# Optimization experiments

Hardware: AMD Instinct MI355X
Metric: run time of the kernel (lower is better)

Reference implementation:

```python
import jax, jax.numpy as jnp
import numpy as np


def setup_inputs() -> dict:
    key = jax.random.key(0)
    kq, kk, kv = jax.random.split(key, 3)
    B, S, D = 4, 4096, 128
    return {
        "q_proj": jax.random.normal(kq, (B, S, D), dtype=jnp.float32),
        "k_proj": jax.random.normal(kk, (B, S, D), dtype=jnp.float32),
        "v_proj": jax.random.normal(kv, (B, S, D), dtype=jnp.float32),
    }


def reference(q_proj, k_proj, v_proj):
    # Block-wise online softmax in the original is mathematically exact
    # full (non-causal) scaled dot-product attention.
    d = q_proj.shape[-1]
    scale = 1.0 / jnp.sqrt(jnp.asarray(d, dtype=q_proj.dtype))
    logits = jnp.einsum('bqd,bkd->bqk', q_proj, k_proj) * scale  # [B,S,S]
    attn = jax.nn.softmax(logits, axis=-1)
    return jnp.einsum('bqk,bkd->bqd', attn, v_proj)
```

## Files before the change

kernel.cpp:

```cpp
#include <hip/hip_runtime.h>
#include <hip/hip_bf16.h>
#include <stdint.h>

#define Bn 4
#define Sn 4096
#define Dn 128
#define SCALE ((float)(0.08838834764831843 * 1.4426950408889634))

typedef __attribute__((ext_vector_type(8)))  short short8;
typedef __attribute__((ext_vector_type(4)))  short short4v;
typedef __attribute__((ext_vector_type(4)))  float f32x4;
typedef __attribute__((ext_vector_type(16))) float f32x16;
typedef __attribute__((ext_vector_type(2)))  uint32_t uint2v;

__device__ __forceinline__ uint32_t bfround(float f){
  union { float f; uint32_t u; } a; a.f = f;
  return a.u + 0x7FFFu + ((a.u >> 16) & 1u);
}
__device__ __forceinline__ uint32_t f2bf2(float lo, float hi){
  return (bfround(hi) & 0xFFFF0000u) | (bfround(lo) >> 16);
}
__device__ __forceinline__ uint32_t f2bf2_fast(float lo, float hi){
  const uint32_t a = __float_as_uint(lo) + 0x8000u;
  const uint32_t b = __float_as_uint(hi) + 0x8000u;
  return __builtin_amdgcn_perm(b, a, 0x07060302u);
}
__device__ __forceinline__ float bf2f(short s){
  union { uint32_t u; float f; } a; a.u = ((uint32_t)(unsigned short)s) << 16; return a.f;
}
__device__ __forceinline__ float fexp2(float x){
#if __has_builtin(__builtin_amdgcn_exp2f)
  return __builtin_amdgcn_exp2f(x);
#else
  return exp2f(x);
#endif
}

__device__ __forceinline__ void gload16(const void* g, void* l){
  __builtin_amdgcn_global_load_lds(
      (const __attribute__((address_space(1))) unsigned int*)g,
      (__attribute__((address_space(3))) unsigned int*)l, 16, 0, 0);
}

__global__ void prep_kernel(const float* __restrict__ k, const float* __restrict__ v,
                            short* __restrict__ kb, short* __restrict__ vt){
  const int bid = blockIdx.x;
  const int t   = threadIdx.x;
  if (bid < 512){
    const int b = bid >> 7, i = bid & 127;
#pragma unroll
    for (int it=0; it<2; ++it){
      const int lin = it*256 + t;
      const int ln = lin & 31;
      const int tg = lin >> 5;
      const int tt = tg >> 1, hh = tg & 1;
      const float* src = k + ((size_t)(b*Sn + i*32 + ln))*Dn + tg*8;
      const f32x4 a = *(const f32x4*)src;
      const f32x4 c = *(const f32x4*)(src + 4);
      union { uint32_t u[4]; short8 s; } pk;
      pk.u[0] = f2bf2(a[0], a[1]);
      pk.u[1] = f2bf2(a[2], a[3]);
      pk.u[2] = f2bf2(c[0], c[1]);
      pk.u[3] = f2bf2(c[2], c[3]);
      *(short8*)(kb + (((size_t)(b*128 + i)*8 + tt)*64 + (hh*32 + ln))*8) = pk.s;
    }
  } else {
    __shared__ float tile[64][65];
    const int vb = bid - 512;
    const int s0 = (vb & 63) * 64;
    const int d0 = ((vb >> 6) & 1) * 64;
    const int b  = vb >> 7;
#pragma unroll
    for (int i=0;i<16;++i){
      int lin = i*256 + t;
      int r = lin >> 6, c = lin & 63;
      tile[r][c] = v[((size_t)(b*Sn + s0 + r))*Dn + d0 + c];
    }
    __syncthreads();
#pragma unroll
    for (int i=0;i<2;++i){
      int lin = i*256 + t;
      int r = lin >> 3;
      int u = lin & 7;
      union { uint32_t w[4]; short8 s; } pk;
#pragma unroll
      for (int p=0;p<4;++p){
        int x0 = u*8 + 2*p, x1 = x0 + 1;
        int k0 = (x0 & ~15) | ((x0 & 3) | (((x0>>2)&1)<<3) | (((x0>>3)&1)<<2));
        int k1 = (x1 & ~15) | ((x1 & 3) | (((x1>>2)&1)<<3) | (((x1>>3)&1)<<2));
        pk.w[p] = f2bf2(tile[k0][r], tile[k1][r]);
      }
      *(short8*)(vt + ((size_t)(b*Dn + d0 + r))*Sn + s0 + u*8) = pk.s;
    }
  }
}

__global__ __launch_bounds__(256, 2) void fa_kernel(
    const float* __restrict__ Qg, const short* __restrict__ Kb,
    const short* __restrict__ VTb, short* __restrict__ parts,
    float* __restrict__ lparts){
  __shared__ __align__(16) char lds[16384];
  const int tid = threadIdx.x;
  const int w = tid >> 6, lane = tid & 63;
  const int ln = lane & 31, h5 = lane >> 5;
  const int idx = blockIdx.x;
  const int b   = idx & 3;
  const int u2  = idx >> 2;
  const int qt  = u2 & 31;
  const int ks  = u2 >> 5;
  const int q0  = qt * 128;
  const int start_it = ks * 32;
  const int n_it     = 32;

  short8 Qf[8];
  {
    const float* qp = Qg + ((size_t)(b*Sn + q0 + w*32 + ln))*Dn;
#pragma unroll
    for (int t=0;t<8;++t){
      const int d0 = t*16 + h5*8;
      const f32x4 a = *(const f32x4*)(qp + d0);
      const f32x4 c = *(const f32x4*)(qp + d0 + 4);
      union { uint32_t u[4]; short8 s; } pk;
      pk.u[0] = f2bf2(a[0]*SCALE, a[1]*SCALE);
      pk.u[1] = f2bf2(a[2]*SCALE, a[3]*SCALE);
      pk.u[2] = f2bf2(c[0]*SCALE, c[1]*SCALE);
      pk.u[3] = f2bf2(c[2]*SCALE, c[3]*SCALE);
      Qf[t] = pk.s;
    }
  }

  f32x16 Ot[4];
#pragma unroll
  for (int m=0;m<4;++m)
#pragma unroll
    for (int r=0;r<16;++r) Ot[m][r] = 0.0f;
  float ls0=0.f, ls1=0.f, ls2=0.f, ls3=0.f;

  int soff[2], doff[2];
  {
#pragma unroll
    for (int u=0;u<2;++u){
      const int ch = w*128 + u*64 + lane;
      const int r  = ch >> 2;
      const int gc = (ch & 3) ^ ((r >> 1) & 3);
      soff[u] = r*8192 + gc*16;
      doff[u] = ch*16;
    }
  }
  const char* gbaseV = (const char*)VTb + (size_t)b*Dn*Sn*2 + (size_t)start_it*64;
  const short* Kbase = Kb + (size_t)(b*128 + start_it)*4096 + (size_t)lane*8;

  auto stage = [&](int i, int ph){
    char* ldsb = lds + ph*8192;
    const char* gb = gbaseV + (size_t)i*64;
#pragma unroll
    for (int u=0;u<2;++u) gload16(gb + soff[u], ldsb + doff[u]);
  };

  auto loadK = [&](short8 (&kf)[8], int i){
    const short* Kp = Kbase + (size_t)i*4096;
#pragma unroll
    for (int t=0;t<8;++t) kf[t] = *(const short8*)(Kp + t*512);
  };

  auto body = [&](const short8 (&kf)[8], const char* bV){
    f32x16 St;
#pragma unroll
    for (int r=0;r<16;++r) St[r] = 0.0f;
    __builtin_amdgcn_s_setprio(1);
#pragma unroll
    for (int t=0;t<8;++t)
      St = __builtin_amdgcn_mfma_f32_32x32x16_bf16(kf[t], Qf[t], St, 0, 0, 0);
    __builtin_amdgcn_s_setprio(0);

#pragma unroll
    for (int r=0;r<16;++r) St[r] = fexp2(St[r]);
#pragma unroll
    for (int r=0;r<16;r+=4){
      ls0 += St[r]; ls1 += St[r+1]; ls2 += St[r+2]; ls3 += St[r+3];
    }

    __builtin_amdgcn_s_setprio(1);
#pragma unroll
    for (int t=0;t<2;++t){
      union { uint32_t u[4]; short8 s; } pf;
      pf.u[0] = f2bf2_fast(St[8*t+0], St[8*t+1]);
      pf.u[1] = f2bf2_fast(St[8*t+2], St[8*t+3]);
      pf.u[2] = f2bf2_fast(St[8*t+4], St[8*t+5]);
      pf.u[3] = f2bf2_fast(St[8*t+6], St[8*t+7]);
      const int phys = ((2*t + h5) ^ ((ln >> 1) & 3)) * 16;
#pragma unroll
      for (int mt=0;mt<4;++mt){
        const short8 vf = *(const short8*)(bV + (size_t)(mt*32+ln)*64 + phys);
        Ot[mt] = __builtin_amdgcn_mfma_f32_32x32x16_bf16(vf, pf.s, Ot[mt], 0, 0, 0);
      }
    }
    __builtin_amdgcn_s_setprio(0);
  };

  short8 kfA[8], kfB[8];
  loadK(kfA, 0);
  stage(0, 0);

  for (int i=0; i<n_it; i+=2){
    __syncthreads();
    stage(i+1, 1);
    loadK(kfB, i+1);
    body(kfA, lds);

    __syncthreads();
    if (i+2 < n_it){ stage(i+2, 0); loadK(kfA, i+2); }
    body(kfB, lds + 8192);
  }

  float lsum = (ls0 + ls1) + (ls2 + ls3);
  lsum += __shfl_xor(lsum, 32, 64);

  const int pslot = (b*32 + qt)*4 + ks;
  short* pbase = parts + (size_t)pslot*16384 + (size_t)(w*32 + ln)*128;
#pragma unroll
  for (int mt=0;mt<4;++mt){
#pragma unroll
    for (int g=0;g<4;++g){
      union { uint32_t u[2]; short4v s; } o;
      o.u[0] = f2bf2(Ot[mt][4*g],   Ot[mt][4*g+1]);
      o.u[1] = f2bf2(Ot[mt][4*g+2], Ot[mt][4*g+3]);
      *(short4v*)(pbase + mt*32 + 8*g + 4*h5) = o.s;
    }
  }
  if (h5 == 0) lparts[(size_t)pslot*128 + w*32 + ln] = lsum;
}

__global__ void reduce_kernel(const short* __restrict__ parts,
                              const float* __restrict__ lparts,
                              float* __restrict__ out){
  const int t  = threadIdx.x;
  const int s  = blockIdx.x >> 3;
  const int qg = (blockIdx.x & 7)*16 + (t >> 4);
  const int d0 = (t & 15) * 8;
  float acc[8];
#pragma unroll
  for (int j=0;j<8;++j) acc[j] = 0.0f;
  float lsum = 0.0f;
#pragma unroll
  for (int ks=0;ks<4;++ks){
    const short8 p = *(const short8*)(parts + ((size_t)(s*4+ks))*16384 + (size_t)qg*128 + d0);
#pragma unroll
    for (int j=0;j<8;++j) acc[j] += bf2f(p[j]);
    lsum += lparts[(size_t)(s*4+ks)*128 + qg];
  }
  const float linv = 1.0f / lsum;
  f32x4 o0, o1;
#pragma unroll
  for (int j=0;j<4;++j){ o0[j] = acc[j]*linv; o1[j] = acc[4+j]*linv; }
  float* op = out + ((size_t)(s*128 + qg))*128 + d0;
  *(f32x4*)op = o0;
  *(f32x4*)(op + 4) = o1;
}

extern "C" void kernel_launch(void* const* d_in, const int* in_sizes, int n_in,
                              void* d_out, int out_size, void* d_ws, size_t ws_size,
                              hipStream_t stream){
  const float* q = (const float*)d_in[0];
  const float* k = (const float*)d_in[1];
  const float* v = (const float*)d_in[2];
  float* out = (float*)d_out;
  char* ws = (char*)d_ws;
  short* kb     = (short*)ws;
  short* vt     = kb + (size_t)Bn*Sn*Dn;
  short* parts  = (short*)(ws + 8388608);
  float* lparts = (float*)(ws + 8388608 + 16777216);

  prep_kernel<<<1024, 256, 0, stream>>>(k, v, kb, vt);
  fa_kernel<<<512, 256, 0, stream>>>(q, kb, vt, parts, lparts);
  reduce_kernel<<<1024, 256, 0, stream>>>(parts, lparts, out);
}
```

Baseline: 121.0 us.

## Pre-swizzle V into MFMA fragment layout and load directly to registers, dropping LDS

The prep kernel now writes V in per-lane MFMA operand fragment order, matching how K is already stored. The attention kernel then loads V fragments straight from global memory into registers, replacing the LDS staging with global_load_lds and the block-wide __syncthreads. Next-iteration K and V loads are issued right after their use, fenced by sched_barriers, as a simple software pipeline. Each wave now fetches all of V itself, with no sharing through LDS, so global/L2 traffic rises and register pressure grows from holding the kf and vf fragment arrays.

```diff
diff --git a/kernel.cpp b/kernel.cpp
--- a/kernel.cpp
+++ b/kernel.cpp
@@ -36,14 +36,8 @@
 #endif
 }
 
-__device__ __forceinline__ void gload16(const void* g, void* l){
-  __builtin_amdgcn_global_load_lds(
-      (const __attribute__((address_space(1))) unsigned int*)g,
-      (__attribute__((address_space(3))) unsigned int*)l, 16, 0, 0);
-}
-
 __global__ void prep_kernel(const float* __restrict__ k, const float* __restrict__ v,
-                            short* __restrict__ kb, short* __restrict__ vt){
+                            short* __restrict__ kb, short* __restrict__ vf){
   const int bid = blockIdx.x;
   const int t   = threadIdx.x;
   if (bid < 512){
@@ -65,41 +59,46 @@
       *(short8*)(kb + (((size_t)(b*128 + i)*8 + tt)*64 + (hh*32 + ln))*8) = pk.s;
     }
   } else {
-    __shared__ float tile[64][65];
+    __shared__ float tile[32][132];
     const int vb = bid - 512;
-    const int s0 = (vb & 63) * 64;
-    const int d0 = ((vb >> 6) & 1) * 64;
-    const int b  = vb >> 7;
-#pragma unroll
-    for (int i=0;i<16;++i){
-      int lin = i*256 + t;
-      int r = lin >> 6, c = lin & 63;
-      tile[r][c] = v[((size_t)(b*Sn + s0 + r))*Dn + d0 + c];
+    const int b = vb >> 7, i = vb & 127;
+#pragma unroll
+    for (int it=0; it<4; ++it){
+      const int lin = it*256 + t;
+      const int row = lin >> 5;
+      const int c4  = lin & 31;
+      const f32x4 val = *(const f32x4*)(v + ((size_t)(b*Sn + i*32 + row))*Dn + c4*4);
+      tile[row][c4*4+0] = val[0];
+      tile[row][c4*4+1] = val[1];
+      tile[row][c4*4+2] = val[2];
+      tile[row][c4*4+3] = val[3];
     }
     __syncthreads();
 #pragma unroll
-    for (int i=0;i<2;++i){
-      int lin = i*256 + t;
-      int r = lin >> 3;
-      int u = lin & 7;
-      union { uint32_t w[4]; short8 s; } pk;
+    for (int cc=0; cc<2; ++cc){
+      const int c = cc*256 + t;
+      const int l = c & 63, fidx = c >> 6;
+      const int t_ = fidx >> 2, mt = fidx & 3;
+      const int ln = l & 31, h5 = l >> 5;
+      const int d = mt*32 + ln;
+      const int kb0 = 16*t_ + 4*h5;
+      union { uint32_t u[4]; short8 s; } pk;
 #pragma unroll
       for (int p=0;p<4;++p){
-        int x0 = u*8 + 2*p, x1 = x0 + 1;
-        int k0 = (x0 & ~15) | ((x0 & 3) | (((x0>>2)&1)<<3) | (((x0>>3)&1)<<2));
-        int k1 = (x1 & ~15) | ((x1 & 3) | (((x1>>2)&1)<<3) | (((x1>>3)&1)<<2));
-        pk.w[p] = f2bf2(tile[k0][r], tile[k1][r]);
+        const int j0 = 2*p, j1 = 2*p+1;
+        const int kl0 = kb0 + (j0&3) + 8*(j0>>2);
+        const int kl1 = kb0 + (j1&3) + 8*(j1>>2);
+        pk.u[p] = f2bf2(tile[kl0][d], tile[kl1][d]);
       }
-      *(short8*)(vt + ((size_t)(b*Dn + d0 + r))*Sn + s0 + u*8) = pk.s;
+      *(short8*)(vf + (((size_t)(b*128 + i)*8 + fidx)*64 + l)*8) = pk.s;
     }
   }
 }
 
 __global__ __launch_bounds__(256, 2) void fa_kernel(
     const float* __restrict__ Qg, const short* __restrict__ Kb,
-    const short* __restrict__ VTb, short* __restrict__ parts,
+    const short* __restrict__ VFb, short* __restrict__ parts,
     float* __restrict__ lparts){
-  __shared__ __align__(16) char lds[16384];
   const int tid = threadIdx.x;
   const int w = tid >> 6, lane = tid & 63;
   const int ln = lane & 31, h5 = lane >> 5;
@@ -136,34 +135,18 @@
     for (int r=0;r<16;++r) Ot[m][r] = 0.0f;
   float ls0=0.f, ls1=0.f, ls2=0.f, ls3=0.f;
 
-  int soff[2], doff[2];
+  const short* Kbase = Kb  + (size_t)(b*128 + start_it)*4096 + (size_t)lane*8;
+  const short* Vbase = VFb + (size_t)(b*128 + start_it)*4096 + (size_t)lane*8;
+
+  short8 kf[8], vf[8];
   {
 #pragma unroll
-    for (int u=0;u<2;++u){
-      const int ch = w*128 + u*64 + lane;
-      const int r  = ch >> 2;
-      const int gc = (ch & 3) ^ ((r >> 1) & 3);
-      soff[u] = r*8192 + gc*16;
-      doff[u] = ch*16;
-    }
-  }
-  const char* gbaseV = (const char*)VTb + (size_t)b*Dn*Sn*2 + (size_t)start_it*64;
-  const short* Kbase = Kb + (size_t)(b*128 + start_it)*4096 + (size_t)lane*8;
-
-  auto stage = [&](int i, int ph){
-    char* ldsb = lds + ph*8192;
-    const char* gb = gbaseV + (size_t)i*64;
-#pragma unroll
-    for (int u=0;u<2;++u) gload16(gb + soff[u], ldsb + doff[u]);
-  };
-
-  auto loadK = [&](short8 (&kf)[8], int i){
-    const short* Kp = Kbase + (size_t)i*4096;
-#pragma unroll
-    for (int t=0;t<8;++t) kf[t] = *(const short8*)(Kp + t*512);
-  };
-
-  auto body = [&](const short8 (&kf)[8], const char* bV){
+    for (int t=0;t<8;++t) kf[t] = *(const short8*)(Kbase + t*512);
+#pragma unroll
+    for (int t=0;t<8;++t) vf[t] = *(const short8*)(Vbase + t*512);
+  }
+
+  for (int i=0; i<n_it; ++i){
     f32x16 St;
 #pragma unroll
     for (int r=0;r<16;++r) St[r] = 0.0f;
@@ -173,6 +156,13 @@
       St = __builtin_amdgcn_mfma_f32_32x32x16_bf16(kf[t], Qf[t], St, 0, 0, 0);
     __builtin_amdgcn_s_setprio(0);
 
+    {
+      const short* Kp = Kbase + (size_t)(i+1)*4096;
+#pragma unroll
+      for (int t=0;t<8;++t) kf[t] = *(const short8*)(Kp + t*512);
+    }
+    __builtin_amdgcn_sched_barrier(0);
+
 #pragma unroll
     for (int r=0;r<16;++r) St[r] = fexp2(St[r]);
 #pragma unroll
@@ -180,37 +170,31 @@
       ls0 += St[r]; ls1 += St[r+1]; ls2 += St[r+2]; ls3 += St[r+3];
     }
 
+    union { uint32_t u[4]; short8 s; } pf0, pf1;
+    pf0.u[0] = f2bf2_fast(St[0], St[1]);
+    pf0.u[1] = f2bf2_fast(St[2], St[3]);
+    pf0.u[2] = f2bf2_fast(St[4], St[5]);
+    pf0.u[3] = f2bf2_fast(St[6], St[7]);
+    pf1.u[0] = f2bf2_fast(St[8], St[9]);
+    pf1.u[1] = f2bf2_fast(St[10], St[11]);
+    pf1.u[2] = f2bf2_fast(St[12], St[13]);
+    pf1.u[3] = f2bf2_fast(St[14], St[15]);
+
     __builtin_amdgcn_s_setprio(1);
 #pragma unroll
-    for (int t=0;t<2;++t){
-      union { uint32_t u[4]; short8 s; } pf;
-      pf.u[0] = f2bf2_fast(St[8*t+0], St[8*t+1]);
-      pf.u[1] = f2bf2_fast(St[8*t+2], St[8*t+3]);
-      pf.u[2] = f2bf2_fast(St[8*t+4], St[8*t+5]);
-      pf.u[3] = f2bf2_fast(St[8*t+6], St[8*t+7]);
-      const int phys = ((2*t + h5) ^ ((ln >> 1) & 3)) * 16;
-#pragma unroll
-      for (int mt=0;mt<4;++mt){
-        const short8 vf = *(const short8*)(bV + (size_t)(mt*32+ln)*64 + phys);
-        Ot[mt] = __builtin_amdgcn_mfma_f32_32x32x16_bf16(vf, pf.s, Ot[mt], 0, 0, 0);
-      }
-    }
+    for (int mt=0;mt<4;++mt)
+      Ot[mt] = __builtin_amdgcn_mfma_f32_32x32x16_bf16(vf[mt],   pf0.s, Ot[mt], 0, 0, 0);
+#pragma unroll
+    for (int mt=0;mt<4;++mt)
+      Ot[mt] = __builtin_amdgcn_mfma_f32_32x32x16_bf16(vf[4+mt], pf1.s, Ot[mt], 0, 0, 0);
     __builtin_amdgcn_s_setprio(0);
-  };
-
-  short8 kfA[8], kfB[8];
-  loadK(kfA, 0);
-  stage(0, 0);
-
-  for (int i=0; i<n_it; i+=2){
-    __syncthreads();
-    stage(i+1, 1);
-    loadK(kfB, i+1);
-    body(kfA, lds);
-
-    __syncthreads();
-    if (i+2 < n_it){ stage(i+2, 0); loadK(kfA, i+2); }
-    body(kfB, lds + 8192);
+
+    {
+      const short* Vp = Vbase + (size_t)(i+1)*4096;
+#pragma unroll
+      for (int t=0;t<8;++t) vf[t] = *(const short8*)(Vp + t*512);
+    }
+    __builtin_amdgcn_sched_barrier(0);
   }
 
   float lsum = (ls0 + ls1) + (ls2 + ls3);
@@ -267,11 +251,11 @@
   float* out = (float*)d_out;
   char* ws = (char*)d_ws;
   short* kb     = (short*)ws;
-  short* vt     = kb + (size_t)Bn*Sn*Dn;
+  short* vfb    = kb + (size_t)Bn*Sn*Dn;
   short* parts  = (short*)(ws + 8388608);
   float* lparts = (float*)(ws + 8388608 + 16777216);
 
-  prep_kernel<<<1024, 256, 0, stream>>>(k, v, kb, vt);
-  fa_kernel<<<512, 256, 0, stream>>>(q, kb, vt, parts, lparts);
+  prep_kernel<<<1024, 256, 0, stream>>>(k, v, kb, vfb);
+  fa_kernel<<<512, 256, 0, stream>>>(q, kb, vfb, parts, lparts);
   reduce_kernel<<<1024, 256, 0, stream>>>(parts, lparts, out);
 }
```

New measurement: 122.7 us. About the same (+1.4%).
